# Kernel optimization log

Measured on AMD Instinct MI355X. Metric: run time of the kernel, lower is better.

The kernel has to match this reference:

```python
import jax, jax.numpy as jnp
import numpy as np

B, Q, T, C = 32, 900, 300, 256
W_CLASS, W_BBOX, W_GIOU, W_CUTIN = 1.0, 5.0, 2.0, 2.0


def _make_boxes(key, shape):
    # valid xyxy boxes: x2>x1, y2>y1
    k1, k2 = jax.random.split(key)
    xy = jax.random.uniform(k1, shape[:-1] + (2,), minval=0.0, maxval=0.6)
    wh = jax.random.uniform(k2, shape[:-1] + (2,), minval=0.05, maxval=0.4)
    return jnp.concatenate([xy, xy + wh], axis=-1).astype(jnp.float32)


def setup_inputs() -> dict:
    key = jax.random.key(0)
    ks = jax.random.split(key, 6)
    return {
        "pred_logits": jax.random.normal(ks[0], (B, Q, C), jnp.float32),
        "pred_boxes": _make_boxes(ks[1], (B, Q, 4)),
        "pred_cutin": jax.random.uniform(ks[2], (B, Q), jnp.float32),
        "tgt_labels": jax.random.randint(ks[3], (B, T), 0, C),
        "tgt_boxes": _make_boxes(ks[4], (B, T, 4)),
        "tgt_cutin": jax.random.uniform(ks[5], (B, T), jnp.float32),
    }


def _cost_matrix(pred_logits, pred_boxes, pred_cutin, tgt_labels, tgt_boxes, tgt_cutin):
    # [B,Q,C] -> class probabilities
    prob = jax.nn.softmax(pred_logits, axis=-1)
    # gather prob at target labels: [B,Q,T]
    idx = jnp.broadcast_to(tgt_labels[:, None, :], (prob.shape[0], prob.shape[1], tgt_labels.shape[1]))
    cost_class = -jnp.take_along_axis(prob, idx, axis=2)

    pb = pred_boxes[:, :, None, :]   # [B,Q,1,4]
    tb = tgt_boxes[:, None, :, :]    # [B,1,T,4]
    # L1 cdist [B,Q,T]
    cost_bbox = jnp.abs(pb - tb).sum(-1)

    # generalized IoU (xyxy), matching torchvision.ops.generalized_box_iou
    area_p = (pred_boxes[..., 2] - pred_boxes[..., 0]) * (pred_boxes[..., 3] - pred_boxes[..., 1])  # [B,Q]
    area_t = (tgt_boxes[..., 2] - tgt_boxes[..., 0]) * (tgt_boxes[..., 3] - tgt_boxes[..., 1])      # [B,T]
    lt = jnp.maximum(pb[..., :2], tb[..., :2])
    rb = jnp.minimum(pb[..., 2:], tb[..., 2:])
    inter = jnp.clip(rb - lt, 0.0).prod(-1)                      # [B,Q,T]
    union = area_p[:, :, None] + area_t[:, None, :] - inter
    iou = inter / union
    lt_e = jnp.minimum(pb[..., :2], tb[..., :2])
    rb_e = jnp.maximum(pb[..., 2:], tb[..., 2:])
    enc = jnp.clip(rb_e - lt_e, 0.0).prod(-1)
    giou = iou - (enc - union) / enc

    cost_cutin = jnp.abs(pred_cutin[:, :, None] - tgt_cutin[:, None, :])

    return W_BBOX * cost_bbox + W_CLASS * cost_class - W_GIOU * giou + W_CUTIN * cost_cutin


_cost_matrix_jit = jax.jit(_cost_matrix)


def _lsa(cost):
    """Jonker-Volgenant shortest-augmenting-path (e-maxx Hungarian).
    cost: (n, m) numpy float64 with n <= m. Returns col assigned to each row.
    Optimal assignment identical in cost to scipy.optimize.linear_sum_assignment."""
    cost = np.asarray(cost, dtype=np.float64)
    n, m = cost.shape
    u = np.zeros(n + 1)
    v = np.zeros(m + 1)
    p = np.zeros(m + 1, dtype=np.int64)    # p[j]: row (1-based) matched to col j
    way = np.zeros(m + 1, dtype=np.int64)
    for i in range(1, n + 1):
        p[0] = i
        j0 = 0
        minv = np.full(m + 1, np.inf)
        used = np.zeros(m + 1, dtype=bool)
        while True:
            used[j0] = True
            i0 = p[j0]
            cur = cost[i0 - 1] - u[i0] - v[1:]
            free = ~used[1:]
            better = free & (cur < minv[1:])
            minv[1:] = np.where(better, cur, minv[1:])
            way[1:] = np.where(better, j0, way[1:])
            masked = np.where(free, minv[1:], np.inf)
            j1 = int(np.argmin(masked)) + 1
            delta = masked[j1 - 1]
            uidx = np.nonzero(used)[0]
            u[p[uidx]] += delta
            v[uidx] -= delta
            minv[1:] = np.where(free, minv[1:] - delta, minv[1:])
            j0 = j1
            if p[j0] == 0:
                break
        while j0:
            j1 = way[j0]
            p[j0] = p[j1]
            j0 = j1
    row2col = np.zeros(n, dtype=np.int64)
    for j in range(1, m + 1):
        if p[j] > 0:
            row2col[p[j] - 1] = j - 1
    return row2col


def reference(pred_logits, pred_boxes, pred_cutin, tgt_labels, tgt_boxes, tgt_cutin):
    Cmat = _cost_matrix_jit(pred_logits, pred_boxes, pred_cutin, tgt_labels, tgt_boxes, tgt_cutin)
    Cnp = np.asarray(Cmat)
    bs, nq, nt = Cnp.shape
    # per-image Hungarian on the transposed (T x Q) cost: each target gets a query.
    q_idx = np.stack([_lsa(Cnp[b].T) for b in range(bs)])         # [B,T] query index per target
    t_idx = np.broadcast_to(np.arange(nt, dtype=np.int64), q_idx.shape).copy()
    return Cmat, jnp.asarray(q_idx), jnp.asarray(t_idx)
```

## Files before the change

kernel.cpp:

```cpp
#include <hip/hip_runtime.h>
#include <float.h>

#define BB 32
#define QQ 900
#define TT 300
#define CC 256

__global__ __launch_bounds__(256)
void softmax_stats_kernel(const float* __restrict__ logits, float2* __restrict__ stats)
{
    const int row = blockIdx.x;
    const float* L = logits + (size_t)row * CC;
    const int tid = threadIdx.x;
    float x = L[tid];

    __shared__ float sredm[4];
    __shared__ float sreds[4];

    float m = x;
    #pragma unroll
    for (int off = 32; off > 0; off >>= 1)
        m = fmaxf(m, __shfl_down(m, off, 64));
    if ((tid & 63) == 0) sredm[tid >> 6] = m;
    __syncthreads();
    m = fmaxf(fmaxf(sredm[0], sredm[1]), fmaxf(sredm[2], sredm[3]));

    float s = expf(x - m);
    #pragma unroll
    for (int off = 32; off > 0; off >>= 1)
        s += __shfl_down(s, off, 64);
    if ((tid & 63) == 0) sreds[tid >> 6] = s;
    __syncthreads();
    if (tid == 0)
        stats[row] = make_float2(m, sreds[0] + sreds[1] + sreds[2] + sreds[3]);
}

__global__ __launch_bounds__(256)
void cost_kernel(const float* __restrict__ logits,
                 const float* __restrict__ pboxes,
                 const float* __restrict__ pcut,
                 const int*   __restrict__ tlabels,
                 const float* __restrict__ tboxes,
                 const float* __restrict__ tcut,
                 const float2* __restrict__ stats,
                 float* __restrict__ Cmat,
                 float* __restrict__ CT,
                 unsigned long long* __restrict__ rowkey)
{
    const int b  = blockIdx.z;
    const int q0 = blockIdx.x * 32;
    const int t0 = blockIdx.y * 32;
    const int tid = threadIdx.x;

    __shared__ float s_pb[32][4], s_tb[32][4];
    __shared__ float s_pc[32], s_tc[32], s_pm[32], s_ps[32], s_pa[32], s_ta[32];
    __shared__ int   s_tl[32];
    __shared__ float s_tile[32][33];

    if (tid < 32) {
        int q = q0 + tid;
        if (q < QQ) {
            const float* pb = pboxes + ((size_t)b * QQ + q) * 4;
            float x1 = pb[0], y1 = pb[1], x2 = pb[2], y2 = pb[3];
            s_pb[tid][0] = x1; s_pb[tid][1] = y1; s_pb[tid][2] = x2; s_pb[tid][3] = y2;
            s_pa[tid] = (x2 - x1) * (y2 - y1);
            s_pc[tid] = pcut[(size_t)b * QQ + q];
            float2 st = stats[(size_t)b * QQ + q];
            s_pm[tid] = st.x; s_ps[tid] = st.y;
        }
    } else if (tid < 64) {
        int tl = tid - 32;
        int t = t0 + tl;
        if (t < TT) {
            const float* tb = tboxes + ((size_t)b * TT + t) * 4;
            float x1 = tb[0], y1 = tb[1], x2 = tb[2], y2 = tb[3];
            s_tb[tl][0] = x1; s_tb[tl][1] = y1; s_tb[tl][2] = x2; s_tb[tl][3] = y2;
            s_ta[tl] = (x2 - x1) * (y2 - y1);
            s_tc[tl] = tcut[(size_t)b * TT + t];
            s_tl[tl] = tlabels[(size_t)b * TT + t];
        }
    }
    __syncthreads();

    const int tl = tid & 31;
    const int t  = t0 + tl;
    #pragma unroll
    for (int k = 0; k < 4; ++k) {
        int ql = (tid >> 5) + 8 * k;
        int q  = q0 + ql;
        if (q < QQ && t < TT) {
            float lg = logits[((size_t)b * QQ + q) * CC + s_tl[tl]];
            float cclass = -(expf(lg - s_pm[ql]) / s_ps[ql]);

            float px1 = s_pb[ql][0], py1 = s_pb[ql][1], px2 = s_pb[ql][2], py2 = s_pb[ql][3];
            float tx1 = s_tb[tl][0], ty1 = s_tb[tl][1], tx2 = s_tb[tl][2], ty2 = s_tb[tl][3];

            float l1 = fabsf(px1 - tx1) + fabsf(py1 - ty1) + fabsf(px2 - tx2) + fabsf(py2 - ty2);

            float iw = fmaxf(fminf(px2, tx2) - fmaxf(px1, tx1), 0.0f);
            float ih = fmaxf(fminf(py2, ty2) - fmaxf(py1, ty1), 0.0f);
            float inter = iw * ih;
            float uni = s_pa[ql] + s_ta[tl] - inter;
            float iou = inter / uni;

            float ew = fmaxf(fmaxf(px2, tx2) - fminf(px1, tx1), 0.0f);
            float eh = fmaxf(fmaxf(py2, ty2) - fminf(py1, ty1), 0.0f);
            float enc = ew * eh;
            float giou = iou - (enc - uni) / enc;

            float cost = 5.0f * l1 + cclass - 2.0f * giou
                       + 2.0f * fabsf(s_pc[ql] - s_tc[tl]);

            Cmat[((size_t)b * QQ + q) * TT + t] = cost;
            s_tile[ql][tl] = cost;
        }
    }
    __syncthreads();

    if (CT != nullptr) {
        #pragma unroll
        for (int k = 0; k < 4; ++k) {
            int tl2 = (tid >> 5) + 8 * k;
            int ql2 = tid & 31;
            int t2 = t0 + tl2, q2 = q0 + ql2;
            if (q2 < QQ && t2 < TT)
                CT[((size_t)b * TT + t2) * QQ + q2] = s_tile[ql2][tl2];
        }
    }

    if (tid < 32) {
        int t2 = t0 + tid;
        if (t2 < TT) {
            int qmax = (QQ - q0 < 32) ? (QQ - q0) : 32;
            unsigned long long best = ~0ull;
            for (int ql2 = 0; ql2 < qmax; ++ql2) {
                unsigned ub = __float_as_uint(s_tile[ql2][tid]);
                unsigned mono = (ub & 0x80000000u) ? ~ub : (ub | 0x80000000u);
                unsigned long long key = ((unsigned long long)mono << 10)
                                       | (unsigned)(q0 + ql2);
                if (key < best) best = key;
            }
            atomicMin(&rowkey[(size_t)b * TT + t2], best);
        }
    }
}

#define STH 256
#define NW (STH / 64)
#define KCOLS 4
#define MLOW ((1ull << 19) - 1ull)

__device__ __forceinline__ unsigned long long monoKey(double x) {
    unsigned long long ub = (unsigned long long)__double_as_longlong(x);
    return (ub & 0x8000000000000000ull) ? ~ub : (ub | 0x8000000000000000ull);
}
__device__ __forceinline__ double unmonoKey(unsigned long long m) {
    unsigned long long ub = (m >> 63) ? (m & 0x7FFFFFFFFFFFFFFFull) : ~m;
    return __longlong_as_double((long long)ub);
}

__device__ __forceinline__ unsigned wave_min_u32(unsigned x) {
    unsigned t;
    t = (unsigned)__builtin_amdgcn_update_dpp((int)x, (int)x, 0x111, 0xf, 0xf, false);
    x = (x < t) ? x : t;
    t = (unsigned)__builtin_amdgcn_update_dpp((int)x, (int)x, 0x112, 0xf, 0xf, false);
    x = (x < t) ? x : t;
    t = (unsigned)__builtin_amdgcn_update_dpp((int)x, (int)x, 0x114, 0xf, 0xf, false);
    x = (x < t) ? x : t;
    t = (unsigned)__builtin_amdgcn_update_dpp((int)x, (int)x, 0x118, 0xf, 0xf, false);
    x = (x < t) ? x : t;
    t = (unsigned)__builtin_amdgcn_update_dpp((int)x, (int)x, 0x142, 0xa, 0xf, false);
    x = (x < t) ? x : t;
    t = (unsigned)__builtin_amdgcn_update_dpp((int)x, (int)x, 0x143, 0xc, 0xf, false);
    x = (x < t) ? x : t;
    return (unsigned)__builtin_amdgcn_readlane((int)x, 63);
}

__global__ __launch_bounds__(STH)
void lsa_kernel(const float* __restrict__ Mbase,
                long long batchStride, long long rowStride, long long colStride,
                const unsigned long long* __restrict__ rowkey,
                float* __restrict__ outq, float* __restrict__ outt)
{
    const int b = blockIdx.x;
    const float* M = Mbase + (size_t)b * batchStride;
    const int tid = threadIdx.x;

    __shared__ double u0[TT + 1];
    __shared__ double v0[QQ + 1];
    __shared__ int    p[QQ + 1];
    __shared__ int    way[QQ + 1];
    __shared__ int    claim[QQ + 1];
    __shared__ int    freeRows[TT];
    __shared__ int    usedList[TT + 1];
    __shared__ double Dent[TT + 1];
    __shared__ unsigned long long redK[2][NW];
    __shared__ int    waveBase[NW];
    __shared__ int    chunkBase;

    for (int j = tid; j <= QQ; j += STH) { v0[j] = 0.0; p[j] = 0; way[j] = 0; claim[j] = 0x7FFFFFFF; }
    for (int i = tid + 1; i <= TT; i += STH) {
        unsigned long long rk = rowkey[(size_t)b * TT + i - 1];
        unsigned mono = (unsigned)(rk >> 10);
        unsigned ub = (mono & 0x80000000u) ? (mono & 0x7FFFFFFFu) : ~mono;
        u0[i] = (double)__uint_as_float(ub);
    }
    if (tid == 0) chunkBase = 0;
    __syncthreads();

    for (int i = tid + 1; i <= TT; i += STH)
        atomicMin(&claim[(int)(rowkey[(size_t)b * TT + i - 1] & 1023ull) + 1], i);
    __syncthreads();

    for (int r = 0; r < (TT + STH - 1) / STH; ++r) {
        int i = tid + r * STH + 1;
        bool lose = false;
        if (i <= TT) {
            int j = (int)(rowkey[(size_t)b * TT + i - 1] & 1023ull) + 1;
            if (claim[j] == i) p[j] = i; else lose = true;
        }
        unsigned long long mk = __ballot(lose);
        int lane = tid & 63, w = tid >> 6;
        int lanePre = __popcll(mk & ((1ull << lane) - 1ull));
        if (lane == 0) waveBase[w] = __popcll(mk);
        __syncthreads();
        if (tid == 0) {
            int acc = chunkBase;
            for (int w2 = 0; w2 < NW; ++w2) { int c = waveBase[w2]; waveBase[w2] = acc; acc += c; }
            chunkBase = acc;
        }
        __syncthreads();
        if (lose) freeRows[waveBase[w] + lanePre] = i;
        __syncthreads();
    }
    const int nFree = chunkBase;

    const int c0 = 4 * tid;
    const bool vec = (colStride == 1) && (c0 < QQ);

    int par = 0;
    for (int f = 0; f < nFree; ++f) {
        const int i = freeRows[f];

        unsigned long long sv[KCOLS];
        double v0r[KCOLS];
        int own[KCOLS];
        bool valid[KCOLS];
        #pragma unroll
        for (int k = 0; k < KCOLS; ++k) {
            int c = c0 + k; int j = c + 1;
            valid[k] = (c < QQ);
            sv[k] = ~0ull;
            v0r[k] = valid[k] ? v0[j] : 0.0;
            own[k] = valid[k] ? p[j] : 0;
        }
        unsigned usedMask = 0;
        int cnt = 1; double D = 0.0; int i0 = i; int j0 = 0; int j1free;

        while (true) {
            const float* Mrow = M + (long long)(i0 - 1) * rowStride;
            float mload[KCOLS];
            if (vec) {
                float4 mv = *reinterpret_cast<const float4*>(Mrow + c0);
                mload[0] = mv.x; mload[1] = mv.y; mload[2] = mv.z; mload[3] = mv.w;
            } else {
                #pragma unroll
                for (int k = 0; k < KCOLS; ++k)
                    mload[k] = valid[k] ? Mrow[(long long)(c0 + k) * colStride] : 0.0f;
            }
            const double base = D - u0[i0];

            unsigned long long bk = ~0ull;
            #pragma unroll
            for (int k = 0; k < KCOLS; ++k) {
                if (valid[k] && !((usedMask >> k) & 1u)) {
                    int j = c0 + k + 1;
                    double cur = (double)mload[k] + (base - v0r[k]);
                    unsigned long long key = (monoKey(cur) & ~MLOW)
                                           | ((unsigned long long)j << 9)
                                           | (unsigned long long)own[k];
                    if (key < sv[k]) { sv[k] = key; way[j] = j0; }
                    if (sv[k] < bk) bk = sv[k];
                }
            }
            {
                unsigned hi = (unsigned)(bk >> 32);
                unsigned lo = (unsigned)(bk & 0xFFFFFFFFull);
                unsigned mhi = wave_min_u32(hi);
                unsigned lo2 = (hi == mhi) ? lo : 0xFFFFFFFFu;
                unsigned mlo = wave_min_u32(lo2);
                if ((tid & 63) == 0)
                    redK[par][tid >> 6] = ((unsigned long long)mhi << 32) | mlo;
            }
            __syncthreads();
            unsigned long long kmin = redK[par][0];
            #pragma unroll
            for (int w = 1; w < NW; ++w) {
                unsigned long long o = redK[par][w];
                if (o < kmin) kmin = o;
            }
            par ^= 1;

            D = unmonoKey(kmin & ~MLOW);
            int j1 = (int)((kmin >> 9) & 1023ull);
            int i1 = (int)(kmin & 511ull);
            if (i1 == 0) { j1free = j1; break; }

            int cj = j1 - 1;
            if ((cj >> 2) == tid) usedMask |= 1u << (cj & 3);
            if (tid == 0) { usedList[cnt] = j1; Dent[cnt] = D; }
            cnt++;
            j0 = j1; i0 = i1;
        }

        __syncthreads();

        for (int k = tid; k < cnt; k += STH) {
            if (k == 0) {
                u0[i] += D;
            } else {
                int ju = usedList[k];
                double d = D - Dent[k];
                u0[p[ju]] += d;
                v0[ju]    -= d;
            }
        }
        __syncthreads();

        if (tid == 0) {
            int jj = j1free;
            while (jj) {
                int jn = way[jj];
                p[jj] = (jn == 0) ? i : p[jn];
                jj = jn;
            }
        }
        __syncthreads();
    }

    for (int j = tid + 1; j <= QQ; j += STH) {
        int pi = p[j];
        if (pi > 0) outq[(size_t)b * TT + (pi - 1)] = (float)(j - 1);
    }
    for (int t = tid; t < TT; t += STH)
        outt[(size_t)b * TT + t] = (float)t;
}

extern "C" void kernel_launch(void* const* d_in, const int* in_sizes, int n_in,
                              void* d_out, int out_size, void* d_ws, size_t ws_size,
                              hipStream_t stream)
{
    const float* logits  = (const float*)d_in[0];
    const float* pboxes  = (const float*)d_in[1];
    const float* pcut    = (const float*)d_in[2];
    const int*   tlabels = (const int*)d_in[3];
    const float* tboxes  = (const float*)d_in[4];
    const float* tcut    = (const float*)d_in[5];

    float* out  = (float*)d_out;
    float* Cmat = out;
    float* outq = out + (size_t)BB * QQ * TT;
    float* outt = outq + (size_t)BB * TT;

    const size_t statsBytes = (size_t)BB * QQ * sizeof(float2);
    const size_t rkBytes    = (size_t)BB * TT * sizeof(unsigned long long);
    const size_t ctBytes    = (size_t)BB * TT * QQ * sizeof(float);

    float2* stats = (float2*)d_ws;
    unsigned long long* rowkey = (unsigned long long*)((char*)d_ws + statsBytes);
    char*   ctPtr = (char*)d_ws + statsBytes + rkBytes;
    bool haveCT = (ws_size >= statsBytes + rkBytes + ctBytes);
    float* CT = haveCT ? (float*)ctPtr : nullptr;

    hipMemsetAsync(rowkey, 0xFF, rkBytes, stream);

    softmax_stats_kernel<<<BB * QQ, 256, 0, stream>>>(logits, stats);

    dim3 grid((QQ + 31) / 32, (TT + 31) / 32, BB);
    cost_kernel<<<grid, 256, 0, stream>>>(logits, pboxes, pcut, tlabels, tboxes,
                                          tcut, stats, Cmat, CT, rowkey);

    if (haveCT) {
        lsa_kernel<<<BB, STH, 0, stream>>>(
            CT, (long long)TT * QQ, (long long)QQ, 1LL, rowkey, outq, outt);
    } else {
        lsa_kernel<<<BB, STH, 0, stream>>>(
            Cmat, (long long)QQ * TT, 1LL, (long long)TT, rowkey, outq, outt);
    }
}
```

Measured before the change: 272.4 us.

## Speculatively prefetch next augmenting-path row and keep column duals in registers

Inside the Hungarian shortest-path loop, each thread now loads the candidate next cost-matrix rows for all four wave winners right after the barrier, before the final min is known, and picks the matching one. This hides the global-memory latency of the serial row fetch. The next free row is also prefetched before the update phase. Column duals v0 move from shared memory into per-thread registers, updated by scanning the used list, and row ownership tags are precomputed. In exchange the kernel issues three extra loads per step and adds a serial per-thread loop over the path length.

New measurement: 280.9 us. +3.1%, slower.

```diff
diff --git a/kernel.cpp b/kernel.cpp
--- a/kernel.cpp
+++ b/kernel.cpp
@@ -187,8 +187,7 @@
     const int tid = threadIdx.x;
 
     __shared__ double u0[TT + 1];
-    __shared__ double v0[QQ + 1];
-    __shared__ int    p[QQ + 1];
+    __shared__ __align__(16) int pcol[QQ];
     __shared__ int    way[QQ + 1];
     __shared__ int    claim[QQ + 1];
     __shared__ int    freeRows[TT];
@@ -198,7 +197,8 @@
     __shared__ int    waveBase[NW];
     __shared__ int    chunkBase;
 
-    for (int j = tid; j <= QQ; j += STH) { v0[j] = 0.0; p[j] = 0; way[j] = 0; claim[j] = 0x7FFFFFFF; }
+    for (int j = tid; j <= QQ; j += STH) { way[j] = 0; claim[j] = 0x7FFFFFFF; }
+    for (int c = tid; c < QQ; c += STH) pcol[c] = 0;
     for (int i = tid + 1; i <= TT; i += STH) {
         unsigned long long rk = rowkey[(size_t)b * TT + i - 1];
         unsigned mono = (unsigned)(rk >> 10);
@@ -217,7 +217,7 @@
         bool lose = false;
         if (i <= TT) {
             int j = (int)(rowkey[(size_t)b * TT + i - 1] & 1023ull) + 1;
-            if (claim[j] == i) p[j] = i; else lose = true;
+            if (claim[j] == i) pcol[j - 1] = i; else lose = true;
         }
         unsigned long long mk = __ballot(lose);
         int lane = tid & 63, w = tid >> 6;
@@ -238,32 +238,49 @@
     const int c0 = 4 * tid;
     const bool vec = (colStride == 1) && (c0 < QQ);
 
+    double v0r[KCOLS] = {0.0, 0.0, 0.0, 0.0};
+    bool valid[KCOLS];
+    #pragma unroll
+    for (int k = 0; k < KCOLS; ++k) valid[k] = (c0 + k < QQ);
+
+    float4 pre4 = make_float4(0.f, 0.f, 0.f, 0.f);
+    if (vec && nFree > 0)
+        pre4 = *reinterpret_cast<const float4*>(M + (long long)(freeRows[0] - 1) * rowStride + c0);
+
     int par = 0;
     for (int f = 0; f < nFree; ++f) {
         const int i = freeRows[f];
 
+        unsigned long long tag[KCOLS];
+        {
+            int own[KCOLS] = {0, 0, 0, 0};
+            if (vec) {
+                int4 pv = *reinterpret_cast<const int4*>(&pcol[c0]);
+                own[0] = pv.x; own[1] = pv.y; own[2] = pv.z; own[3] = pv.w;
+            } else {
+                #pragma unroll
+                for (int k = 0; k < KCOLS; ++k)
+                    if (valid[k]) own[k] = pcol[c0 + k];
+            }
+            #pragma unroll
+            for (int k = 0; k < KCOLS; ++k)
+                tag[k] = ((unsigned long long)(c0 + k + 1) << 9)
+                       | (unsigned long long)own[k];
+        }
+
         unsigned long long sv[KCOLS];
-        double v0r[KCOLS];
-        int own[KCOLS];
-        bool valid[KCOLS];
         #pragma unroll
-        for (int k = 0; k < KCOLS; ++k) {
-            int c = c0 + k; int j = c + 1;
-            valid[k] = (c < QQ);
-            sv[k] = ~0ull;
-            v0r[k] = valid[k] ? v0[j] : 0.0;
-            own[k] = valid[k] ? p[j] : 0;
-        }
+        for (int k = 0; k < KCOLS; ++k) sv[k] = ~0ull;
         unsigned usedMask = 0;
         int cnt = 1; double D = 0.0; int i0 = i; int j0 = 0; int j1free;
+        float4 cur4 = pre4;
 
         while (true) {
-            const float* Mrow = M + (long long)(i0 - 1) * rowStride;
             float mload[KCOLS];
             if (vec) {
-                float4 mv = *reinterpret_cast<const float4*>(Mrow + c0);
-                mload[0] = mv.x; mload[1] = mv.y; mload[2] = mv.z; mload[3] = mv.w;
+                mload[0] = cur4.x; mload[1] = cur4.y; mload[2] = cur4.z; mload[3] = cur4.w;
             } else {
+                const float* Mrow = M + (long long)(i0 - 1) * rowStride;
                 #pragma unroll
                 for (int k = 0; k < KCOLS; ++k)
                     mload[k] = valid[k] ? Mrow[(long long)(c0 + k) * colStride] : 0.0f;
@@ -274,12 +291,9 @@
             #pragma unroll
             for (int k = 0; k < KCOLS; ++k) {
                 if (valid[k] && !((usedMask >> k) & 1u)) {
-                    int j = c0 + k + 1;
                     double cur = (double)mload[k] + (base - v0r[k]);
-                    unsigned long long key = (monoKey(cur) & ~MLOW)
-                                           | ((unsigned long long)j << 9)
-                                           | (unsigned long long)own[k];
-                    if (key < sv[k]) { sv[k] = key; way[j] = j0; }
+                    unsigned long long key = (monoKey(cur) & ~MLOW) | tag[k];
+                    if (key < sv[k]) { sv[k] = key; way[c0 + k + 1] = j0; }
                     if (sv[k] < bk) bk = sv[k];
                 }
             }
@@ -293,18 +307,35 @@
                     redK[par][tid >> 6] = ((unsigned long long)mhi << 32) | mlo;
             }
             __syncthreads();
-            unsigned long long kmin = redK[par][0];
-            #pragma unroll
-            for (int w = 1; w < NW; ++w) {
-                unsigned long long o = redK[par][w];
-                if (o < kmin) kmin = o;
-            }
+
+            unsigned long long k0 = redK[par][0], k1 = redK[par][1];
+            unsigned long long k2 = redK[par][2], k3 = redK[par][3];
+
+            float4 p0, p1, p2, p3;
+            if (vec) {
+                int r0 = (int)(k0 & 511ull), r1 = (int)(k1 & 511ull);
+                int r2 = (int)(k2 & 511ull), r3 = (int)(k3 & 511ull);
+                r0 = (r0 > 0) ? r0 - 1 : 0;  r1 = (r1 > 0) ? r1 - 1 : 0;
+                r2 = (r2 > 0) ? r2 - 1 : 0;  r3 = (r3 > 0) ? r3 - 1 : 0;
+                p0 = *reinterpret_cast<const float4*>(M + (long long)r0 * rowStride + c0);
+                p1 = *reinterpret_cast<const float4*>(M + (long long)r1 * rowStride + c0);
+                p2 = *reinterpret_cast<const float4*>(M + (long long)r2 * rowStride + c0);
+                p3 = *reinterpret_cast<const float4*>(M + (long long)r3 * rowStride + c0);
+            }
+
+            unsigned long long kmin = k0;
+            if (k1 < kmin) kmin = k1;
+            if (k2 < kmin) kmin = k2;
+            if (k3 < kmin) kmin = k3;
             par ^= 1;
 
             D = unmonoKey(kmin & ~MLOW);
             int j1 = (int)((kmin >> 9) & 1023ull);
             int i1 = (int)(kmin & 511ull);
             if (i1 == 0) { j1free = j1; break; }
+
+            if (vec)
+                cur4 = (kmin == k0) ? p0 : (kmin == k1) ? p1 : (kmin == k2) ? p2 : p3;
 
             int cj = j1 - 1;
             if ((cj >> 2) == tid) usedMask |= 1u << (cj & 3);
@@ -313,16 +344,24 @@
             j0 = j1; i0 = i1;
         }
 
-        __syncthreads();
-
+        if (vec && f + 1 < nFree)
+            pre4 = *reinterpret_cast<const float4*>(
+                M + (long long)(freeRows[f + 1] - 1) * rowStride + c0);
+
+        __syncthreads();
+
+        for (int k = 1; k < cnt; ++k) {
+            int ju = usedList[k];
+            double d = D - Dent[k];
+            int rel = ju - 1 - c0;
+            if (rel >= 0 && rel < KCOLS) v0r[rel] -= d;
+        }
         for (int k = tid; k < cnt; k += STH) {
             if (k == 0) {
                 u0[i] += D;
             } else {
                 int ju = usedList[k];
-                double d = D - Dent[k];
-                u0[p[ju]] += d;
-                v0[ju]    -= d;
+                u0[pcol[ju - 1]] += D - Dent[k];
             }
         }
         __syncthreads();
@@ -331,16 +370,16 @@
             int jj = j1free;
             while (jj) {
                 int jn = way[jj];
-                p[jj] = (jn == 0) ? i : p[jn];
+                pcol[jj - 1] = (jn == 0) ? i : pcol[jn - 1];
                 jj = jn;
             }
         }
         __syncthreads();
     }
 
-    for (int j = tid + 1; j <= QQ; j += STH) {
-        int pi = p[j];
-        if (pi > 0) outq[(size_t)b * TT + (pi - 1)] = (float)(j - 1);
+    for (int c = tid; c < QQ; c += STH) {
+        int pi = pcol[c];
+        if (pi > 0) outq[(size_t)b * TT + (pi - 1)] = (float)c;
     }
     for (int t = tid; t < TT; t += STH)
         outt[(size_t)b * TT + t] = (float)t;
```
